# Optimization experiments

Measured on AMD Instinct MI355X. Metric: run time of the kernel, lower is better.

The kernel has to match this reference:

```python
import jax, jax.numpy as jnp
import numpy as np

E, NSRC, NDST = 1_000_000, 100_000, 100_000
D = 128  # efeat_dim = src_dim = dst_dim = hidden_dim = output_dim
LN_EPS = 1e-5


def setup_inputs() -> dict:
    key = jax.random.key(0)
    ks = jax.random.split(key, 12)
    s = 1.0 / np.sqrt(3 * D)  # fan_in of the original concat Linear is 3*D
    so = 1.0 / np.sqrt(D)
    return {
        "efeat": jax.random.normal(ks[0], (E, D), jnp.float32),
        "src_feat": jax.random.normal(ks[1], (NSRC, D), jnp.float32),
        "dst_feat": jax.random.normal(ks[2], (NDST, D), jnp.float32),
        "src_idx": jax.random.randint(ks[3], (E,), 0, NSRC, jnp.int32),
        "dst_idx": jax.random.randint(ks[4], (E,), 0, NDST, jnp.int32),
        "w_efeat": jax.random.uniform(ks[5], (D, D), jnp.float32, -s, s),
        "w_src": jax.random.uniform(ks[6], (D, D), jnp.float32, -s, s),
        "w_dst": jax.random.uniform(ks[7], (D, D), jnp.float32, -s, s),
        "b0": jax.random.uniform(ks[8], (D,), jnp.float32, -s, s),
        "w_out": jax.random.uniform(ks[9], (D, D), jnp.float32, -so, so),
        "b_out": jax.random.uniform(ks[10], (D,), jnp.float32, -so, so),
        "ln_g": jnp.ones((D,), jnp.float32),
        "ln_b": jnp.zeros((D,), jnp.float32),
    }


def reference(efeat, src_feat, dst_feat, src_idx, dst_idx,
              w_efeat, w_src, w_dst, b0, w_out, b_out, ln_g, ln_b):
    # Per-node linears first (cheap, [N, D]), then irregular gather to edges.
    mlp_src = src_feat @ w_src.T                 # [Nsrc, D]
    mlp_dst = dst_feat @ w_dst.T + b0            # [Ndst, D] (bias lives here)
    # update_efeat_bipartite_e2e(mode='sum'): gather + elementwise sum per edge
    h = efeat @ w_efeat.T + mlp_src[src_idx] + mlp_dst[dst_idx]  # [E, D]
    # MLP stack: SiLU -> Linear -> LayerNorm (hidden_layers=1)
    h = jax.nn.silu(h)
    y = h @ w_out.T + b_out                      # [E, D]
    mu = jnp.mean(y, axis=-1, keepdims=True)
    var = jnp.mean(jnp.square(y - mu), axis=-1, keepdims=True)
    return (y - mu) * jax.lax.rsqrt(var + LN_EPS) * ln_g + ln_b
```

## Files before the change

### kernel.cpp

```cpp
#include <hip/hip_runtime.h>
#include <hip/hip_bf16.h>

#define DDIM 128

typedef float    f32x16 __attribute__((ext_vector_type(16)));
typedef float    f32x4  __attribute__((ext_vector_type(4)));
typedef short    bf16x8 __attribute__((ext_vector_type(8)));
typedef __bf16   bf16x2t __attribute__((ext_vector_type(2)));
typedef unsigned u32x2  __attribute__((ext_vector_type(2)));
typedef unsigned u32x4  __attribute__((ext_vector_type(4)));
typedef unsigned short us4 __attribute__((ext_vector_type(4)));
typedef unsigned short us8 __attribute__((ext_vector_type(8)));

__device__ __forceinline__ unsigned pkbf(float a, float b) {
    bf16x2t v; v[0] = (__bf16)a; v[1] = (__bf16)b;
    return __builtin_bit_cast(unsigned, v);
}

__device__ __forceinline__ short f2bf16s(float a) {
    __bf16 b = (__bf16)a;
    return __builtin_bit_cast(short, b);
}

__device__ __forceinline__ float bf16tof(unsigned short u) {
    return __builtin_bit_cast(float, ((unsigned)u) << 16);
}

__device__ __forceinline__ bf16x8 cvt8(f32x4 a, f32x4 b) {
    u32x4 u = { pkbf(a[0],a[1]), pkbf(a[2],a[3]), pkbf(b[0],b[1]), pkbf(b[2],b[3]) };
    return __builtin_bit_cast(bf16x8, u);
}

__device__ __forceinline__ void plswap(unsigned &x, unsigned &y) {
    u32x2 r = __builtin_amdgcn_permlane32_swap(x, y, false, false);
    x = r[0]; y = r[1];
}

__device__ __forceinline__ float silu(float x) {
    return x * __builtin_amdgcn_rcpf(1.0f + __expf(-x));
}

__device__ __forceinline__ void load_lds16(const void* g, void* l) {
    __builtin_amdgcn_global_load_lds(
        (const __attribute__((address_space(1))) void*)g,
        (__attribute__((address_space(3))) void*)l, 16, 0, 0);
}

__global__ void prep_weights(const float* __restrict__ we, const float* __restrict__ wsrc,
                             const float* __restrict__ wdst, const float* __restrict__ wout,
                             short* __restrict__ w1frag, short* __restrict__ w2frag) {
    int tid = blockIdx.x * 256 + threadIdx.x;
    if (tid < 24 * 128 * 16) {
        int k8 = tid & 7;
        int hi = (tid >> 3) & 1;
        int n  = (tid >> 4) & 127;
        int s  = tid >> 11;
        int col = 16 * s + 8 * hi + k8;
        const float* src = (col < 128) ? we : ((col < 256) ? wsrc : wdst);
        w1frag[tid] = f2bf16s(src[n * 128 + (col & 127)]);
    } else {
        int t2 = tid - 24 * 128 * 16;
        int k8 = t2 & 7;
        int hi = (t2 >> 3) & 1;
        int n  = (t2 >> 4) & 127;
        int s  = t2 >> 11;
        int col = 16 * s + 8 * hi + k8;
        w2frag[t2] = f2bf16s(wout[n * 128 + col]);
    }
}

__global__ __launch_bounds__(256, 4) void node_table(
    const float* __restrict__ feat, const short* __restrict__ w1frag,
    int segoff, short* __restrict__ tbl, int N)
{
    __shared__ __align__(16) short wl[16384];

    const int tid  = threadIdx.x;
    {
        const us8* s1 = (const us8*)(w1frag + segoff * 2048);
        us8* d1 = (us8*)wl;
        for (int i = tid; i < 2048; i += 256) d1[i] = s1[i];
    }
    __syncthreads();

    const int wave = tid >> 6;
    const int lane = tid & 63;
    const int lo   = lane & 31;
    const int hi   = lane >> 5;
    const int base = blockIdx.x * 128 + wave * 32;
    const int row  = base + lo;
    const int rcl  = row < N ? row : N - 1;
    const float* pn = feat + (size_t)rcl * DDIM;
    const int coff  = 8 * hi;
    const int fslot = (lo * 2 + hi) * 8;

    f32x4 fa[8], fb[8];
#pragma unroll
    for (int s = 0; s < 8; ++s) {
        const f32x4* pv = (const f32x4*)(pn + 16 * s + coff);
        fa[s] = pv[0];
        fb[s] = pv[1];
    }

    f32x16 acc[4];
#pragma unroll
    for (int t = 0; t < 4; ++t)
#pragma unroll
        for (int r = 0; r < 16; ++r) acc[t][r] = 0.0f;

#pragma unroll
    for (int s = 0; s < 8; ++s) {
        bf16x8 a = cvt8(fa[s], fb[s]);
        const short* wb = wl + s * 2048 + fslot;
#pragma unroll
        for (int t = 0; t < 4; ++t) {
            bf16x8 w = *(const bf16x8*)(wb + t * 512);
            acc[t] = __builtin_amdgcn_mfma_f32_32x32x16_bf16(a, w, acc[t], 0, 0, 0);
        }
    }

#pragma unroll
    for (int r = 0; r < 16; ++r) {
        const int m = (r & 3) + 8 * (r >> 2) + 4 * hi;
        const int node = base + m;
        if (node < N) {
            short* po = tbl + (size_t)node * DDIM;
#pragma unroll
            for (int t = 0; t < 4; ++t)
                po[32 * t + lo] = f2bf16s(acc[t][r]);
        }
    }
}

__global__ __launch_bounds__(256, 1) void edge_kernel_dma(
    const float* __restrict__ efeat, const short* __restrict__ tsrc,
    const short* __restrict__ tdst, const int* __restrict__ src_idx,
    const int* __restrict__ dst_idx, const float* __restrict__ b0,
    const float* __restrict__ b_out, const float* __restrict__ ln_g,
    const float* __restrict__ ln_b, const short* __restrict__ w1frag,
    const short* __restrict__ w2frag, float* __restrict__ out, int E)
{
    __shared__ __align__(16) short wlds[32768];
    __shared__ __align__(16) float b0l[128], bol[128], gl[128], bl[128];
    __shared__ __align__(16) char  ebuf_all[4 * 16384];

    const int tid = threadIdx.x;
    {
        const us8* s1 = (const us8*)w1frag;
        us8* d1 = (us8*)wlds;
        for (int i = tid; i < 2048; i += 256) d1[i] = s1[i];
        const us8* s2 = (const us8*)w2frag;
        us8* d2 = (us8*)(wlds + 16384);
        for (int i = tid; i < 2048; i += 256) d2[i] = s2[i];
        if (tid < 128) {
            b0l[tid] = b0[tid];  bol[tid] = b_out[tid];
            gl[tid]  = ln_g[tid]; bl[tid] = ln_b[tid];
        }
    }
    __syncthreads();

    const int wave = tid >> 6;
    const int lane = tid & 63;
    const int lo   = lane & 31;
    const int hi   = lane >> 5;
    const int poff  = 4 * hi;
    const int fslot = (lo * 2 + hi) * 8;
    const int xsw   = lo & 7;

    char* ebuf = ebuf_all + wave * 16384;

    const int wid    = blockIdx.x * 4 + wave;
    const int nwaves = gridDim.x * 4;
    const int stride = nwaves * 32;
    int tb = wid * 32;
    if (tb >= E) return;

    auto stage = [&](int t) {
#pragma unroll
        for (int k = 0; k < 16; ++k) {
            const int r  = 2 * k + hi;
            const int cs = lo ^ (r & 7);
            int gr = t + r; if (gr >= E) gr = E - 1;
            const char* gp = (const char*)(efeat + (size_t)gr * DDIM) + cs * 16;
            load_lds16(gp, ebuf + k * 1024);
        }
    };

    stage(tb);
    __builtin_amdgcn_sched_barrier(0);
    int ecl0 = tb + lo; if (ecl0 >= E) ecl0 = E - 1;
    int si = src_idx[ecl0];
    int di = dst_idx[ecl0];

    for (;;) {
        __builtin_amdgcn_sched_barrier(0);
        const short* prs = tsrc + (size_t)si * DDIM;
        const short* prd = tdst + (size_t)di * DDIM;
        us4 tsv[16], tdv[16];
#pragma unroll
        for (int t = 0; t < 4; ++t)
#pragma unroll
            for (int Q = 0; Q < 4; ++Q) {
                const int c = 32 * t + 8 * Q + poff;
                tsv[t * 4 + Q] = *(const us4*)(prs + c);
                tdv[t * 4 + Q] = *(const us4*)(prd + c);
            }
        __builtin_amdgcn_sched_barrier(0);

        asm volatile("s_waitcnt vmcnt(32)" ::: "memory");
        __builtin_amdgcn_sched_barrier(0);

        f32x16 acc[4];
#pragma unroll
        for (int t = 0; t < 4; ++t)
#pragma unroll
            for (int Q = 0; Q < 4; ++Q) {
                f32x4 bq = *(const f32x4*)(b0l + 32 * t + 8 * Q + poff);
                acc[t][4*Q+0] = bq[0]; acc[t][4*Q+1] = bq[1];
                acc[t][4*Q+2] = bq[2]; acc[t][4*Q+3] = bq[3];
            }

        const char* rb = ebuf + lo * 512;
#pragma unroll
        for (int s = 0; s < 8; ++s) {
            const int g0 = 4 * s + 2 * hi;
            f32x4 fa = *(const f32x4*)(rb + 16 * ((g0    ) ^ xsw));
            f32x4 fb = *(const f32x4*)(rb + 16 * ((g0 + 1) ^ xsw));
            bf16x8 x = cvt8(fa, fb);
            const short* wb = wlds + s * 2048 + fslot;
#pragma unroll
            for (int t = 0; t < 4; ++t) {
                bf16x8 w = *(const bf16x8*)(wb + t * 512);
                acc[t] = __builtin_amdgcn_mfma_f32_32x32x16_bf16(w, x, acc[t], 0, 0, 0);
            }
        }

        asm volatile("s_waitcnt lgkmcnt(0)" ::: "memory");
        __builtin_amdgcn_sched_barrier(0);
        const int nt = tb + stride;
        const bool hasnext = nt < E;
        if (hasnext) {
            stage(nt);
            int ecn = nt + lo; if (ecn >= E) ecn = E - 1;
            si = src_idx[ecn];
            di = dst_idx[ecn];
        }
        __builtin_amdgcn_sched_barrier(0);

#pragma unroll
        for (int t = 0; t < 4; ++t)
#pragma unroll
            for (int Q = 0; Q < 4; ++Q) {
                us4 a = tsv[t * 4 + Q], d = tdv[t * 4 + Q];
#pragma unroll
                for (int j = 0; j < 4; ++j)
                    acc[t][4*Q+j] += bf16tof(a[j]) + bf16tof(d[j]);
            }

        unsigned hbf[4][4][2];
#pragma unroll
        for (int t = 0; t < 4; ++t)
#pragma unroll
            for (int Q = 0; Q < 4; ++Q) {
                float h0 = silu(acc[t][4*Q+0]), h1 = silu(acc[t][4*Q+1]);
                float h2 = silu(acc[t][4*Q+2]), h3 = silu(acc[t][4*Q+3]);
                hbf[t][Q][0] = pkbf(h0, h1);
                hbf[t][Q][1] = pkbf(h2, h3);
            }

        f32x16 acc2[4];
#pragma unroll
        for (int tt = 0; tt < 4; ++tt) {
            float bv = bol[32 * tt + lo];
#pragma unroll
            for (int r = 0; r < 16; ++r) acc2[tt][r] = bv;
        }

#pragma unroll
        for (int s = 0; s < 8; ++s) {
            const int t  = s >> 1;
            const int q0 = (2 * s) & 3;
            const int q1 = q0 + 1;
            unsigned X0 = hbf[t][q0][0], X1 = hbf[t][q0][1];
            unsigned Y0 = hbf[t][q1][0], Y1 = hbf[t][q1][1];
            plswap(X0, Y0);
            plswap(X1, Y1);
            u32x4 fv = { X0, X1, Y0, Y1 };
            bf16x8 hf = __builtin_bit_cast(bf16x8, fv);
            const short* wb = wlds + 16384 + s * 2048 + fslot;
#pragma unroll
            for (int tt = 0; tt < 4; ++tt) {
                bf16x8 w = *(const bf16x8*)(wb + tt * 512);
                acc2[tt] = __builtin_amdgcn_mfma_f32_32x32x16_bf16(hf, w, acc2[tt], 0, 0, 0);
            }
        }

        float gvw[4], bvw[4];
#pragma unroll
        for (int tt = 0; tt < 4; ++tt) {
            gvw[tt] = gl[32 * tt + lo];
            bvw[tt] = bl[32 * tt + lo];
        }

#pragma unroll
        for (int r = 0; r < 16; ++r) {
            float s1 = acc2[0][r] + acc2[1][r] + acc2[2][r] + acc2[3][r];
            float s2 = acc2[0][r]*acc2[0][r] + acc2[1][r]*acc2[1][r]
                     + acc2[2][r]*acc2[2][r] + acc2[3][r]*acc2[3][r];
#pragma unroll
            for (int msk = 1; msk < 32; msk <<= 1) {
                s1 += __shfl_xor(s1, msk, 64);
                s2 += __shfl_xor(s2, msk, 64);
            }
            const float mu   = s1 * (1.0f / 128.0f);
            const float var  = s2 * (1.0f / 128.0f) - mu * mu;
            const float rstd = rsqrtf(var + 1e-5f);
            const int   m    = (r & 3) + 8 * (r >> 2) + 4 * hi;
            const int   eo   = tb + m;
            if (eo < E) {
                float* po = out + (size_t)eo * DDIM;
#pragma unroll
                for (int tt = 0; tt < 4; ++tt) {
                    float o = (acc2[tt][r] - mu) * rstd * gvw[tt] + bvw[tt];
                    po[32 * tt + lo] = o;
                }
            }
        }

        if (!hasnext) break;
        tb = nt;
    }
}

__global__ __launch_bounds__(256, 4) void edge_kernel_fullk(
    const float* __restrict__ efeat, const float* __restrict__ src_feat,
    const float* __restrict__ dst_feat, const int* __restrict__ src_idx,
    const int* __restrict__ dst_idx, const float* __restrict__ b0,
    const float* __restrict__ b_out, const float* __restrict__ ln_g,
    const float* __restrict__ ln_b, const short* __restrict__ w1frag,
    const short* __restrict__ w2frag, float* __restrict__ out, int E)
{
    const int tid  = threadIdx.x;
    const int wave = tid >> 6;
    const int lane = tid & 63;
    const int lo   = lane & 31;
    const int hi   = lane >> 5;
    const int ebase = blockIdx.x * 128 + wave * 32;

    const int erow = ebase + lo;
    const int ecl  = erow < E ? erow : E - 1;
    const int sidx = src_idx[ecl];
    const int didx = dst_idx[ecl];
    const float* pe = efeat    + (size_t)ecl  * DDIM;
    const float* ps = src_feat + (size_t)sidx * DDIM;
    const float* pd = dst_feat + (size_t)didx * DDIM;

    const int coff  = 8 * hi;
    const int poff  = 4 * hi;
    const int fslot = (lo * 2 + hi) * 8;

    float bov[4], gv[4], bv[4];
#pragma unroll
    for (int tt = 0; tt < 4; ++tt) {
        int n = 32 * tt + lo;
        bov[tt] = b_out[n]; gv[tt] = ln_g[n]; bv[tt] = ln_b[n];
    }

    f32x16 acc[4];
#pragma unroll
    for (int t = 0; t < 4; ++t)
#pragma unroll
        for (int Q = 0; Q < 4; ++Q) {
            f32x4 bq = *(const f32x4*)(b0 + 32 * t + 8 * Q + poff);
            acc[t][4*Q+0] = bq[0]; acc[t][4*Q+1] = bq[1];
            acc[t][4*Q+2] = bq[2]; acc[t][4*Q+3] = bq[3];
        }

#pragma unroll
    for (int seg = 0; seg < 3; ++seg) {
        const float* p = (seg == 0) ? pe : ((seg == 1) ? ps : pd);
#pragma unroll
        for (int ks = 0; ks < 8; ++ks) {
            const f32x4* pv = (const f32x4*)(p + 16 * ks + coff);
            f32x4 fa = pv[0], fb = pv[1];
            bf16x8 x = cvt8(fa, fb);
            const int s = seg * 8 + ks;
            const short* wb = w1frag + s * 2048 + fslot;
#pragma unroll
            for (int t = 0; t < 4; ++t) {
                bf16x8 w = *(const bf16x8*)(wb + t * 512);
                acc[t] = __builtin_amdgcn_mfma_f32_32x32x16_bf16(w, x, acc[t], 0, 0, 0);
            }
        }
    }

    unsigned hbf[4][4][2];
#pragma unroll
    for (int t = 0; t < 4; ++t)
#pragma unroll
        for (int Q = 0; Q < 4; ++Q) {
            float h0 = silu(acc[t][4*Q+0]), h1 = silu(acc[t][4*Q+1]);
            float h2 = silu(acc[t][4*Q+2]), h3 = silu(acc[t][4*Q+3]);
            hbf[t][Q][0] = pkbf(h0, h1);
            hbf[t][Q][1] = pkbf(h2, h3);
        }

    f32x16 acc2[4];
#pragma unroll
    for (int tt = 0; tt < 4; ++tt)
#pragma unroll
        for (int r = 0; r < 16; ++r) acc2[tt][r] = bov[tt];

#pragma unroll
    for (int s = 0; s < 8; ++s) {
        const int t  = s >> 1;
        const int q0 = (2 * s) & 3;
        const int q1 = q0 + 1;
        unsigned X0 = hbf[t][q0][0], X1 = hbf[t][q0][1];
        unsigned Y0 = hbf[t][q1][0], Y1 = hbf[t][q1][1];
        plswap(X0, Y0);
        plswap(X1, Y1);
        u32x4 fv = { X0, X1, Y0, Y1 };
        bf16x8 hf = __builtin_bit_cast(bf16x8, fv);
        const short* wb = w2frag + s * 2048 + fslot;
#pragma unroll
        for (int tt = 0; tt < 4; ++tt) {
            bf16x8 w = *(const bf16x8*)(wb + tt * 512);
            acc2[tt] = __builtin_amdgcn_mfma_f32_32x32x16_bf16(hf, w, acc2[tt], 0, 0, 0);
        }
    }

#pragma unroll
    for (int r = 0; r < 16; ++r) {
        float s1 = acc2[0][r] + acc2[1][r] + acc2[2][r] + acc2[3][r];
        float s2 = acc2[0][r]*acc2[0][r] + acc2[1][r]*acc2[1][r]
                 + acc2[2][r]*acc2[2][r] + acc2[3][r]*acc2[3][r];
#pragma unroll
        for (int msk = 1; msk < 32; msk <<= 1) {
            s1 += __shfl_xor(s1, msk, 64);
            s2 += __shfl_xor(s2, msk, 64);
        }
        const float mu   = s1 * (1.0f / 128.0f);
        const float var  = s2 * (1.0f / 128.0f) - mu * mu;
        const float rstd = rsqrtf(var + 1e-5f);
        const int   m    = (r & 3) + 8 * (r >> 2) + 4 * hi;
        const int   eo   = ebase + m;
        if (eo < E) {
            float* po = out + (size_t)eo * DDIM;
#pragma unroll
            for (int tt = 0; tt < 4; ++tt) {
                float o = (acc2[tt][r] - mu) * rstd * gv[tt] + bv[tt];
                po[32 * tt + lo] = o;
            }
        }
    }
}

extern "C" void kernel_launch(void* const* d_in, const int* in_sizes, int n_in,
                              void* d_out, int out_size, void* d_ws, size_t ws_size,
                              hipStream_t stream)
{
    const float* efeat    = (const float*)d_in[0];
    const float* src_feat = (const float*)d_in[1];
    const float* dst_feat = (const float*)d_in[2];
    const int*   src_idx  = (const int*)d_in[3];
    const int*   dst_idx  = (const int*)d_in[4];
    const float* w_efeat  = (const float*)d_in[5];
    const float* w_src    = (const float*)d_in[6];
    const float* w_dst    = (const float*)d_in[7];
    const float* b0       = (const float*)d_in[8];
    const float* w_out    = (const float*)d_in[9];
    const float* b_out    = (const float*)d_in[10];
    const float* ln_g     = (const float*)d_in[11];
    const float* ln_b     = (const float*)d_in[12];
    float* out = (float*)d_out;
    const int E    = in_sizes[3];
    const int nsrc = in_sizes[1] / DDIM;
    const int ndst = in_sizes[2] / DDIM;

    short* w1frag = (short*)d_ws;
    short* w2frag = (short*)((char*)d_ws + 24 * 128 * 16 * 2);
    const size_t tab_off  = 128 * 1024;
    const size_t need_tab = tab_off + ((size_t)nsrc + (size_t)ndst) * DDIM * 2;

    prep_weights<<<256, 256, 0, stream>>>(w_efeat, w_src, w_dst, w_out, w1frag, w2frag);

    if (ws_size >= need_tab) {
        short* tsrc = (short*)((char*)d_ws + tab_off);
        short* tdst = tsrc + (size_t)nsrc * DDIM;
        node_table<<<(nsrc + 127) / 128, 256, 0, stream>>>(src_feat, w1frag, 8,  tsrc, nsrc);
        node_table<<<(ndst + 127) / 128, 256, 0, stream>>>(dst_feat, w1frag, 16, tdst, ndst);
        edge_kernel_dma<<<256, 256, 0, stream>>>(efeat, tsrc, tdst, src_idx, dst_idx,
                                                 b0, b_out, ln_g, ln_b, w1frag, w2frag, out, E);
    } else {
        const int nb = (E + 127) / 128;
        edge_kernel_fullk<<<nb, 256, 0, stream>>>(efeat, src_feat, dst_feat, src_idx, dst_idx,
                                                  b0, b_out, ln_g, ln_b, w1frag, w2frag, out, E);
    }
}
```

Before: 380.2 us.

## Software-pipeline node-feature gathers one tile ahead with ping-pong register buffers

```diff
diff --git a/kernel.cpp b/kernel.cpp
--- a/kernel.cpp
+++ b/kernel.cpp
@@ -185,30 +185,43 @@
             load_lds16(gp, ebuf + k * 1024);
         }
     };
-
-    stage(tb);
-    __builtin_amdgcn_sched_barrier(0);
-    int ecl0 = tb + lo; if (ecl0 >= E) ecl0 = E - 1;
-    int si = src_idx[ecl0];
-    int di = dst_idx[ecl0];
-
-    for (;;) {
-        __builtin_amdgcn_sched_barrier(0);
+    auto load_idx = [&](int t, int& si, int& di) {
+        int ec = t + lo; if (ec >= E) ec = E - 1;
+        si = src_idx[ec]; di = dst_idx[ec];
+    };
+    auto load_gather = [&](int si, int di, us4 (&ts)[16], us4 (&td)[16]) {
         const short* prs = tsrc + (size_t)si * DDIM;
         const short* prd = tdst + (size_t)di * DDIM;
-        us4 tsv[16], tdv[16];
 #pragma unroll
         for (int t = 0; t < 4; ++t)
 #pragma unroll
             for (int Q = 0; Q < 4; ++Q) {
                 const int c = 32 * t + 8 * Q + poff;
-                tsv[t * 4 + Q] = *(const us4*)(prs + c);
-                tdv[t * 4 + Q] = *(const us4*)(prd + c);
-            }
-        __builtin_amdgcn_sched_barrier(0);
-
+                ts[t * 4 + Q] = *(const us4*)(prs + c);
+                td[t * 4 + Q] = *(const us4*)(prd + c);
+            }
+    };
+
+    us4 tsA[16], tdA[16], tsB[16], tdB[16];
+
+    {
+        int si, di;
+        load_idx(tb, si, di);
+        __builtin_amdgcn_sched_barrier(0);
+        stage(tb);
+        __builtin_amdgcn_sched_barrier(0);
+        load_gather(si, di, tsA, tdA);
+        __builtin_amdgcn_sched_barrier(0);
         asm volatile("s_waitcnt vmcnt(32)" ::: "memory");
         __builtin_amdgcn_sched_barrier(0);
+    }
+
+    auto do_tile = [&](int T, us4 (&cts)[16], us4 (&ctd)[16],
+                       us4 (&nts)[16], us4 (&ntd)[16]) -> bool {
+        const int nt = T + stride;
+        const bool hasnext = nt < E;
+        int nsi = 0, ndi = 0;
+        if (hasnext) load_idx(nt, nsi, ndi);
 
         f32x16 acc[4];
 #pragma unroll
@@ -237,25 +250,21 @@
 
         asm volatile("s_waitcnt lgkmcnt(0)" ::: "memory");
         __builtin_amdgcn_sched_barrier(0);
-        const int nt = tb + stride;
-        const bool hasnext = nt < E;
-        if (hasnext) {
-            stage(nt);
-            int ecn = nt + lo; if (ecn >= E) ecn = E - 1;
-            si = src_idx[ecn];
-            di = dst_idx[ecn];
-        }
+        if (hasnext) stage(nt);
         __builtin_amdgcn_sched_barrier(0);
 
 #pragma unroll
         for (int t = 0; t < 4; ++t)
 #pragma unroll
             for (int Q = 0; Q < 4; ++Q) {
-                us4 a = tsv[t * 4 + Q], d = tdv[t * 4 + Q];
+                us4 a = cts[t * 4 + Q], d = ctd[t * 4 + Q];
 #pragma unroll
                 for (int j = 0; j < 4; ++j)
                     acc[t][4*Q+j] += bf16tof(a[j]) + bf16tof(d[j]);
             }
+
+        if (hasnext) load_gather(nsi, ndi, nts, ntd);
+        __builtin_amdgcn_sched_barrier(0);
 
         unsigned hbf[4][4][2];
 #pragma unroll
@@ -316,7 +325,7 @@
             const float var  = s2 * (1.0f / 128.0f) - mu * mu;
             const float rstd = rsqrtf(var + 1e-5f);
             const int   m    = (r & 3) + 8 * (r >> 2) + 4 * hi;
-            const int   eo   = tb + m;
+            const int   eo   = T + m;
             if (eo < E) {
                 float* po = out + (size_t)eo * DDIM;
 #pragma unroll
@@ -327,8 +336,18 @@
             }
         }
 
-        if (!hasnext) break;
-        tb = nt;
+        if (hasnext) {
+            asm volatile("s_waitcnt vmcnt(63)" ::: "memory");
+            __builtin_amdgcn_sched_barrier(0);
+        }
+        return hasnext;
+    };
+
+    for (;;) {
+        if (!do_tile(tb, tsA, tdA, tsB, tdB)) break;
+        tb += stride;
+        if (!do_tile(tb, tsB, tdB, tsA, tdA)) break;
+        tb += stride;
     }
 }
 
```

Result: slower. 403.5 us (+6.1%).
